# Kernel optimization log

Measured on AMD Instinct MI355X. Metric: run time of the kernel, lower is better.

The kernel has to match this reference:

```python
import jax, jax.numpy as jnp
import numpy as np

B, C, H, W = 4, 256, 64, 64
INTER = C // 2
BN_EPS = 1e-5


def setup_inputs() -> dict:
    key = jax.random.key(0)
    ks = jax.random.split(key, 12)
    s = 0.05
    return {
        "x": jax.random.normal(ks[0], (B, C, H, W), dtype=jnp.float32),
        "theta_w": jax.random.normal(ks[1], (INTER, C), dtype=jnp.float32) * s,
        "theta_b": jax.random.normal(ks[2], (INTER,), dtype=jnp.float32) * s,
        "phi_w": jax.random.normal(ks[3], (INTER, C), dtype=jnp.float32) * s,
        "phi_b": jax.random.normal(ks[4], (INTER,), dtype=jnp.float32) * s,
        "g_w": jax.random.normal(ks[5], (INTER, C), dtype=jnp.float32) * s,
        "g_b": jax.random.normal(ks[6], (INTER,), dtype=jnp.float32) * s,
        "W_w": jax.random.normal(ks[7], (C, INTER), dtype=jnp.float32) * s,
        "W_b": jax.random.normal(ks[8], (C,), dtype=jnp.float32) * s,
        "bn_gamma": jnp.ones((C,), dtype=jnp.float32),
        "bn_beta": jnp.zeros((C,), dtype=jnp.float32),
    }


def _conv1x1(x, w, b):
    # 1x1 conv == per-pixel GEMM: (B,C,H,W) x (O,C) -> (B,O,H,W)
    return jnp.einsum("bchw,oc->bohw", x, w) + b[None, :, None, None]


def reference(x, theta_w, theta_b, phi_w, phi_b, g_w, g_b, W_w, W_b, bn_gamma, bn_beta):
    b, c, h, w = x.shape
    hw = h * w
    theta = _conv1x1(x, theta_w, theta_b).reshape(b, -1, hw)  # (B, inter, HW) -> queries
    phi = _conv1x1(x, phi_w, phi_b).reshape(b, -1, hw)        # (B, inter, HW) -> keys
    g = _conv1x1(x, g_w, g_b).reshape(b, -1, hw)              # (B, inter, HW) -> values
    # f[n,m] = <theta[:,n], phi[:,m]> over all HW spatial positions
    f = jnp.einsum("bin,bim->bnm", theta, phi)                # (B, HW, HW)
    attn = jax.nn.softmax(f, axis=-1)
    y = jnp.einsum("bnm,bim->bin", attn, g)                   # (B, inter, HW)
    y = y.reshape(b, c // 2, h, w)
    wy = _conv1x1(y, W_w, W_b)                                # (B, C, H, W)
    # BatchNorm2d (training-mode batch statistics, per channel)
    mean = jnp.mean(wy, axis=(0, 2, 3), keepdims=True)
    var = jnp.var(wy, axis=(0, 2, 3), keepdims=True)
    wy_bn = bn_gamma[None, :, None, None] * (wy - mean) * jax.lax.rsqrt(var + BN_EPS) + bn_beta[None, :, None, None]
    return wy_bn + x
```

## Files before the change

kernel.cpp:

```cpp
#include <hip/hip_runtime.h>
#include <hip/hip_bf16.h>

#define HWN   4096
#define CIN   256
#define NINTER 128
#define NBATCH 4
#define BN_EPS 1e-5f
#define NC    4
#define CHUNK 1024
#define LOG2E 1.4426950408889634f
#define SMAX  64.0f

typedef __bf16 bf16_t;
typedef __bf16 bf16x8 __attribute__((ext_vector_type(8)));
typedef __bf16 bf16x4 __attribute__((ext_vector_type(4)));
typedef float  f32x4  __attribute__((ext_vector_type(4)));
typedef float  f32x16 __attribute__((ext_vector_type(16)));

__device__ __forceinline__ float fexp2(float x) {
  return __builtin_amdgcn_exp2f(x);
}

#define OFF_QH  0
#define OFF_KH  4194304
#define OFF_V   8388608
#define OFF_YH  12582912
#define OFF_OP  16777216
#define OFF_WY  16777216
#define OFF_LP  50331648
#define OFF_WBF 50855936
#define OFF_ST  51380224

__device__ __forceinline__ void split_bf16(float v, bf16_t& h, bf16_t& l) {
  h = (bf16_t)v;
  l = (bf16_t)(v - (float)h);
}

__global__ __launch_bounds__(256) void convert_weights(
    const float* __restrict__ tw, const float* __restrict__ pw,
    const float* __restrict__ gw, const float* __restrict__ ww,
    bf16_t* __restrict__ out) {
  int i = blockIdx.x * 256 + threadIdx.x;
  float v;
  if (i < 32768)        v = tw[i];
  else if (i < 65536)   v = pw[i - 32768];
  else if (i < 98304)   v = gw[i - 65536];
  else                  v = ww[i - 98304];
  bf16_t h, l;
  split_bf16(v, h, l);
  out[i] = h;
  out[131072 + i] = l;
}

__global__ __launch_bounds__(256, 4) void qkv_kernel(
    const float* __restrict__ x, const bf16_t* __restrict__ wbf,
    const float* __restrict__ tb, const float* __restrict__ pb,
    const float* __restrict__ gb,
    bf16_t* __restrict__ Qh, bf16_t* __restrict__ Kh, bf16_t* __restrict__ V) {
  const int ntb  = blockIdx.x;
  const int b    = blockIdx.y;
  const int tid  = threadIdx.x;
  const int lane = tid & 63;
  const int wv   = tid >> 6;
  const int l31  = lane & 31;
  const int half = lane >> 5;

  __shared__ __align__(16) bf16_t smem[4608];
  bf16_t (*xTh)[72] = (bf16_t(*)[72])smem;
  bf16_t (*xTl)[72] = (bf16_t(*)[72])(smem + 2304);
  bf16_t (*Tr)[136] = (bf16_t(*)[136])smem;

  const bf16_t* Th = wbf;
  const bf16_t* Tl = wbf + 131072;
  const bf16_t* Ph = wbf + 32768;
  const bf16_t* Pl = wbf + 131072 + 32768;
  const bf16_t* Gh = wbf + 65536;
  const float*  xb = x + (size_t)b * CIN * HWN + ntb * 32;

  f32x16 aq, ak, av;
#pragma unroll
  for (int i = 0; i < 16; i++) { aq[i] = 0.f; ak[i] = 0.f; av[i] = 0.f; }

  for (int c0 = 0; c0 < 256; c0 += 64) {
    __syncthreads();
#pragma unroll
    for (int i = 0; i < 8; i++) {
      int idx = tid + i * 256;
      int cc = idx >> 5;
      int nn = idx & 31;
      float v = xb[(size_t)(c0 + cc) * HWN + nn];
      bf16_t h, l;
      split_bf16(v, h, l);
      xTh[nn][cc] = h;
      xTl[nn][cc] = l;
    }
    __syncthreads();
#pragma unroll
    for (int kk = 0; kk < 64; kk += 16) {
      size_t woff = (size_t)(32 * wv + l31) * 256 + c0 + kk + half * 8;
      bf16x8 th = *(const bf16x8*)(Th + woff);
      bf16x8 tl = *(const bf16x8*)(Tl + woff);
      bf16x8 ph = *(const bf16x8*)(Ph + woff);
      bf16x8 pl = *(const bf16x8*)(Pl + woff);
      bf16x8 gh = *(const bf16x8*)(Gh + woff);
      bf16x8 bh = *(const bf16x8*)(&xTh[l31][kk + half * 8]);
      bf16x8 bl = *(const bf16x8*)(&xTl[l31][kk + half * 8]);
      aq = __builtin_amdgcn_mfma_f32_32x32x16_bf16(th, bh, aq, 0, 0, 0);
      aq = __builtin_amdgcn_mfma_f32_32x32x16_bf16(th, bl, aq, 0, 0, 0);
      aq = __builtin_amdgcn_mfma_f32_32x32x16_bf16(tl, bh, aq, 0, 0, 0);
      ak = __builtin_amdgcn_mfma_f32_32x32x16_bf16(ph, bh, ak, 0, 0, 0);
      ak = __builtin_amdgcn_mfma_f32_32x32x16_bf16(ph, bl, ak, 0, 0, 0);
      ak = __builtin_amdgcn_mfma_f32_32x32x16_bf16(pl, bh, ak, 0, 0, 0);
      av = __builtin_amdgcn_mfma_f32_32x32x16_bf16(gh, bh, av, 0, 0, 0);
    }
  }

  const int trow = tid >> 3;
  const int tc16 = (tid & 7) * 16;
  bf16_t* qh = Qh + ((size_t)b * HWN + ntb * 32) * NINTER;
  bf16_t* kh = Kh + ((size_t)b * HWN + ntb * 32) * NINTER;

#pragma unroll
  for (int rnd = 0; rnd < 2; rnd++) {
    __syncthreads();
#pragma unroll
    for (int rg = 0; rg < 4; rg++) {
      int och0 = 32 * wv + 8 * rg + 4 * half;
#pragma unroll
      for (int j = 0; j < 4; j++) {
        float v = (rnd == 0) ? (aq[rg * 4 + j] + tb[och0 + j]) * LOG2E
                             : (ak[rg * 4 + j] + pb[och0 + j]);
        Tr[l31][och0 + j] = (bf16_t)v;
      }
    }
    __syncthreads();
    bf16_t* dst = (rnd == 0) ? qh : kh;
    bf16x8 v0 = *(const bf16x8*)(&Tr[trow][tc16]);
    bf16x8 v1 = *(const bf16x8*)(&Tr[trow][tc16 + 8]);
    *(bf16x8*)(dst + (size_t)trow * NINTER + tc16) = v0;
    *(bf16x8*)(dst + (size_t)trow * NINTER + tc16 + 8) = v1;
  }

  const int n = ntb * 32 + l31;
  bf16_t* vd = V + (size_t)b * NINTER * HWN;
#pragma unroll
  for (int r = 0; r < 16; r++) {
    int och = 32 * wv + (r & 3) + 8 * (r >> 2) + 4 * half;
    vd[(size_t)och * HWN + n] = (bf16_t)(av[r] + gb[och]);
  }
}

__global__ __launch_bounds__(256, 2) void attn_kernel(
    const bf16_t* __restrict__ Qh, const bf16_t* __restrict__ Kh,
    const bf16_t* __restrict__ V,
    float* __restrict__ Opart, float* __restrict__ Lp) {
  const int qt    = blockIdx.x;
  const int chunk = blockIdx.y;
  const int b     = blockIdx.z;
  const int tid   = threadIdx.x;
  const int lane  = tid & 63;
  const int wv    = tid >> 6;
  const int l15   = lane & 15;
  const int quad  = lane >> 4;
  const int kbase = chunk * CHUNK;

  __shared__ __align__(16) bf16_t Klds[32][136];
  __shared__ __align__(16) bf16_t Vlds[144][56];
  __shared__ __align__(16) bf16_t Plds[4][32][40];

  const bf16_t* Qhb = Qh + (size_t)b * HWN * NINTER;
  const bf16_t* Khb = Kh + (size_t)b * HWN * NINTER;
  const bf16_t* Vb  = V + (size_t)b * NINTER * HWN;

  if (tid < 112) {
    int row = 128 + tid / 7;
    int c8 = (tid % 7) * 8;
    bf16x8 v;
#pragma unroll
    for (int j = 0; j < 8; j++) v[j] = (bf16_t)((row == 128) ? 1.0f : 0.0f);
    *(bf16x8*)(&Vlds[row][c8]) = v;
  }

  bf16x8 qf[2][4];
#pragma unroll
  for (int qs = 0; qs < 2; qs++) {
    const int qrow = qt * 128 + wv * 32 + qs * 16 + l15;
#pragma unroll
    for (int kc = 0; kc < 4; kc++)
      qf[qs][kc] = *(const bf16x8*)(Qhb + (size_t)qrow * NINTER + kc * 32 + quad * 8);
  }

  f32x4 o[2][8], ol[2];
#pragma unroll
  for (int qs = 0; qs < 2; qs++) {
#pragma unroll
    for (int dt = 0; dt < 8; dt++)
#pragma unroll
      for (int i = 0; i < 4; i++) o[qs][dt][i] = 0.f;
#pragma unroll
    for (int i = 0; i < 4; i++) ol[qs][i] = 0.f;
  }

  for (int t = 0; t < 32; t++) {
    __syncthreads();
#pragma unroll
    for (int i = 0; i < 2; i++) {
      int idx = tid + i * 256;
      int row = idx >> 4;
      int c8 = (idx & 15) * 8;
      *(uint4*)(&Klds[row][c8]) =
          *(const uint4*)(Khb + (size_t)(kbase + t * 32 + row) * NINTER + c8);
    }
#pragma unroll
    for (int i = 0; i < 2; i++) {
      int idx = tid + i * 256;
      int row = idx >> 2;
      int c8 = (idx & 3) * 8;
      *(uint4*)(&Vlds[row][c8]) =
          *(const uint4*)(Vb + (size_t)row * HWN + kbase + t * 32 + c8);
    }
    __syncthreads();

    f32x4 s[2][2];
#pragma unroll
    for (int qs = 0; qs < 2; qs++)
#pragma unroll
      for (int ks = 0; ks < 2; ks++)
#pragma unroll
        for (int i = 0; i < 4; i++) s[qs][ks][i] = 0.f;
#pragma unroll
    for (int ks = 0; ks < 2; ks++)
#pragma unroll
      for (int kc = 0; kc < 4; kc++) {
        bf16x8 kf = *(const bf16x8*)(&Klds[ks * 16 + l15][kc * 32 + quad * 8]);
        s[0][ks] = __builtin_amdgcn_mfma_f32_16x16x32_bf16(qf[0][kc], kf, s[0][ks], 0, 0, 0);
        s[1][ks] = __builtin_amdgcn_mfma_f32_16x16x32_bf16(qf[1][kc], kf, s[1][ks], 0, 0, 0);
      }

#pragma unroll
    for (int qs = 0; qs < 2; qs++)
#pragma unroll
      for (int ks = 0; ks < 2; ks++)
#pragma unroll
        for (int r = 0; r < 4; r++)
          Plds[wv][qs * 16 + quad * 4 + r][ks * 16 + l15] =
              (bf16_t)fexp2(s[qs][ks][r] - SMAX);

    bf16x8 pf0 = *(const bf16x8*)(&Plds[wv][l15][quad * 8]);
    bf16x8 pf1 = *(const bf16x8*)(&Plds[wv][16 + l15][quad * 8]);
#pragma unroll
    for (int dt = 0; dt < 8; dt++) {
      bf16x8 vf = *(const bf16x8*)(&Vlds[dt * 16 + l15][quad * 8]);
      o[0][dt] = __builtin_amdgcn_mfma_f32_16x16x32_bf16(pf0, vf, o[0][dt], 0, 0, 0);
      o[1][dt] = __builtin_amdgcn_mfma_f32_16x16x32_bf16(pf1, vf, o[1][dt], 0, 0, 0);
    }
    bf16x8 vfl = *(const bf16x8*)(&Vlds[128 + l15][quad * 8]);
    ol[0] = __builtin_amdgcn_mfma_f32_16x16x32_bf16(pf0, vfl, ol[0], 0, 0, 0);
    ol[1] = __builtin_amdgcn_mfma_f32_16x16x32_bf16(pf1, vfl, ol[1], 0, 0, 0);
  }

  float* Ob = Opart + ((size_t)(b * NC + chunk) * HWN) * NINTER;
#pragma unroll
  for (int qs = 0; qs < 2; qs++)
#pragma unroll
    for (int r = 0; r < 4; r++) {
      int n = qt * 128 + wv * 32 + qs * 16 + quad * 4 + r;
#pragma unroll
      for (int dt = 0; dt < 8; dt++)
        Ob[(size_t)n * NINTER + dt * 16 + l15] = o[qs][dt][r];
      if (l15 == 0)
        Lp[(size_t)(b * NC + chunk) * HWN + n] = ol[qs][r];
    }
}

__global__ __launch_bounds__(256, 4) void attn_combine(
    const float* __restrict__ Opart, const float* __restrict__ Lp,
    bf16_t* __restrict__ Yh) {
  int gid = blockIdx.x * 256 + threadIdx.x;
  int d8 = gid & 15;
  int n = (gid >> 4) & 4095;
  int b = gid >> 16;

  float lsum = 0.f;
  float acc[8];
#pragma unroll
  for (int j = 0; j < 8; j++) acc[j] = 0.f;
  const f32x4* Op4 = (const f32x4*)Opart;
#pragma unroll
  for (int c = 0; c < NC; c++) {
    lsum += Lp[(size_t)(b * NC + c) * HWN + n];
    f32x4 o0 = Op4[((size_t)(b * NC + c) * HWN + n) * 32 + d8 * 2];
    f32x4 o1 = Op4[((size_t)(b * NC + c) * HWN + n) * 32 + d8 * 2 + 1];
#pragma unroll
    for (int j = 0; j < 4; j++) { acc[j] += o0[j]; acc[4 + j] += o1[j]; }
  }
  float inv = 1.f / lsum;
  bf16x8 y8;
#pragma unroll
  for (int j = 0; j < 8; j++) y8[j] = (bf16_t)(acc[j] * inv);
  *(bf16x8*)(Yh + ((size_t)b * HWN + n) * NINTER + d8 * 8) = y8;
}

__global__ __launch_bounds__(256, 4) void wconv_kernel(
    const bf16_t* __restrict__ Wbf, const bf16_t* __restrict__ Yp,
    const float* __restrict__ Wb, bf16_t* __restrict__ WY) {
  const int ntb = blockIdx.x;
  const int b   = blockIdx.y;
  const int tid = threadIdx.x;
  const int lane = tid & 63;
  const int wv   = tid >> 6;
  const int l31  = lane & 31;
  const int half = lane >> 5;

  const bf16_t* Wh = Wbf + 98304;
  const bf16_t* Yr = Yp + (size_t)b * HWN * NINTER + (size_t)ntb * 32 * NINTER;

  f32x16 acc[2];
#pragma unroll
  for (int c = 0; c < 2; c++)
#pragma unroll
    for (int i = 0; i < 16; i++) acc[c][i] = 0.f;

#pragma unroll
  for (int k0 = 0; k0 < 128; k0 += 16) {
    bf16x8 a0 = *(const bf16x8*)(Wh + (size_t)(wv * 64 + l31) * NINTER + k0 + half * 8);
    bf16x8 a1 = *(const bf16x8*)(Wh + (size_t)(wv * 64 + 32 + l31) * NINTER + k0 + half * 8);
    bf16x8 b0 = *(const bf16x8*)(Yr + (size_t)l31 * NINTER + k0 + half * 8);
    acc[0] = __builtin_amdgcn_mfma_f32_32x32x16_bf16(a0, b0, acc[0], 0, 0, 0);
    acc[1] = __builtin_amdgcn_mfma_f32_32x32x16_bf16(a1, b0, acc[1], 0, 0, 0);
  }

  bf16_t* dst = WY + (size_t)b * 256 * HWN + ntb * 32;
#pragma unroll
  for (int ct = 0; ct < 2; ct++)
#pragma unroll
    for (int r = 0; r < 16; r++) {
      int co = wv * 64 + ct * 32 + (r & 3) + 8 * (r >> 2) + 4 * half;
      dst[(size_t)co * HWN + l31] = (bf16_t)(acc[ct][r] + Wb[co]);
    }
}

__global__ __launch_bounds__(256) void stats_kernel(
    const bf16_t* __restrict__ WY, float* __restrict__ stats) {
  const int c = blockIdx.x;
  const int tid = threadIdx.x;
  float s = 0.f, s2 = 0.f;
  for (int b = 0; b < NBATCH; b++) {
    const bf16_t* p = WY + ((size_t)b * 256 + c) * HWN;
    for (int i = tid * 8; i < HWN; i += 2048) {
      bf16x8 v8 = *(const bf16x8*)(p + i);
#pragma unroll
      for (int j = 0; j < 8; j++) {
        float v = (float)v8[j];
        s += v;
        s2 += v * v;
      }
    }
  }
#pragma unroll
  for (int off = 1; off < 64; off <<= 1) {
    s += __shfl_xor(s, off);
    s2 += __shfl_xor(s2, off);
  }
  __shared__ float red[8];
  int wv = tid >> 6;
  if ((tid & 63) == 0) { red[wv] = s; red[4 + wv] = s2; }
  __syncthreads();
  if (tid == 0) {
    float S = red[0] + red[1] + red[2] + red[3];
    float S2 = red[4] + red[5] + red[6] + red[7];
    float mean = S * (1.f / 16384.f);
    float var = S2 * (1.f / 16384.f) - mean * mean;
    stats[c] = mean;
    stats[256 + c] = rsqrtf(var + BN_EPS);
  }
}

__global__ __launch_bounds__(256) void bn_kernel(
    const bf16_t* __restrict__ WY, const float* __restrict__ x,
    const float* __restrict__ stats, const float* __restrict__ gamma,
    const float* __restrict__ beta, float* __restrict__ out) {
  int idx = blockIdx.x * 256 + threadIdx.x;
  int e = idx * 4;
  int c = (e >> 12) & 255;
  bf16x4 w4 = *(const bf16x4*)(WY + e);
  float4 xv = *(const float4*)(x + e);
  float mean = stats[c];
  float g = gamma[c] * stats[256 + c];
  float bb = beta[c];
  float4 o;
  o.x = g * ((float)w4[0] - mean) + bb + xv.x;
  o.y = g * ((float)w4[1] - mean) + bb + xv.y;
  o.z = g * ((float)w4[2] - mean) + bb + xv.z;
  o.w = g * ((float)w4[3] - mean) + bb + xv.w;
  *(float4*)(out + e) = o;
}

extern "C" void kernel_launch(void* const* d_in, const int* in_sizes, int n_in,
                              void* d_out, int out_size, void* d_ws, size_t ws_size,
                              hipStream_t stream) {
  const float* x       = (const float*)d_in[0];
  const float* theta_b = (const float*)d_in[2];
  const float* phi_b   = (const float*)d_in[4];
  const float* g_b     = (const float*)d_in[6];
  const float* W_b     = (const float*)d_in[8];
  const float* bn_g    = (const float*)d_in[9];
  const float* bn_b    = (const float*)d_in[10];
  float* out = (float*)d_out;

  char* ws = (char*)d_ws;
  bf16_t* Qh  = (bf16_t*)(ws + OFF_QH);
  bf16_t* Kh  = (bf16_t*)(ws + OFF_KH);
  bf16_t* V   = (bf16_t*)(ws + OFF_V);
  bf16_t* Yh  = (bf16_t*)(ws + OFF_YH);
  float*  OP  = (float*)(ws + OFF_OP);
  bf16_t* WY  = (bf16_t*)(ws + OFF_WY);
  float*  LP  = (float*)(ws + OFF_LP);
  bf16_t* WBF = (bf16_t*)(ws + OFF_WBF);
  float*  ST  = (float*)(ws + OFF_ST);

  convert_weights<<<512, 256, 0, stream>>>(
      (const float*)d_in[1], (const float*)d_in[3],
      (const float*)d_in[5], (const float*)d_in[7], WBF);
  qkv_kernel<<<dim3(128, NBATCH), 256, 0, stream>>>(
      x, WBF, theta_b, phi_b, g_b, Qh, Kh, V);
  attn_kernel<<<dim3(32, NC, NBATCH), 256, 0, stream>>>(
      Qh, Kh, V, OP, LP);
  attn_combine<<<1024, 256, 0, stream>>>(OP, LP, Yh);
  wconv_kernel<<<dim3(128, NBATCH), 256, 0, stream>>>(WBF, Yh, W_b, WY);
  stats_kernel<<<256, 256, 0, stream>>>(WY, ST);
  bn_kernel<<<4096, 256, 0, stream>>>(WY, x, ST, bn_g, bn_b, out);
}
```

Measured before the change: 187.7 us.

## Fuse weight conversion, attention combine and BN stats into neighbouring kernels

Drops the separate weight-conversion kernel; qkv and wconv now read fp32 weights and split or convert them to bf16 inline. The attention partial-sum combine moves into wconv through an LDS tile, and the BN statistics are accumulated with atomics in wconv's epilogue, so bn_kernel derives mean and variance itself. This removes three launches and the Yh and stats round trips through memory. The cost is redundant weight conversion in every block, per-row shuffle reductions with many atomics, and atomic ordering that is not deterministic.

```diff
diff --git a/kernel.cpp b/kernel.cpp
--- a/kernel.cpp
+++ b/kernel.cpp
@@ -21,42 +21,52 @@
   return __builtin_amdgcn_exp2f(x);
 }
 
+__device__ __forceinline__ void split_bf16(float v, bf16_t& h, bf16_t& l) {
+  h = (bf16_t)v;
+  l = (bf16_t)(v - (float)h);
+}
+
+__device__ __forceinline__ void load_split8(const float* p, bf16x8& h, bf16x8& l) {
+  f32x4 a = *(const f32x4*)p;
+  f32x4 b = *(const f32x4*)(p + 4);
+#pragma unroll
+  for (int j = 0; j < 4; j++) {
+    bf16_t hh, ll;
+    split_bf16(a[j], hh, ll);
+    h[j] = hh; l[j] = ll;
+    split_bf16(b[j], hh, ll);
+    h[4 + j] = hh; l[4 + j] = ll;
+  }
+}
+
+__device__ __forceinline__ bf16x8 load_cvt8(const float* p) {
+  f32x4 a = *(const f32x4*)p;
+  f32x4 b = *(const f32x4*)(p + 4);
+  bf16x8 r;
+#pragma unroll
+  for (int j = 0; j < 4; j++) {
+    r[j] = (bf16_t)a[j];
+    r[4 + j] = (bf16_t)b[j];
+  }
+  return r;
+}
+
 #define OFF_QH  0
 #define OFF_KH  4194304
 #define OFF_V   8388608
-#define OFF_YH  12582912
-#define OFF_OP  16777216
-#define OFF_WY  16777216
-#define OFF_LP  50331648
-#define OFF_WBF 50855936
-#define OFF_ST  51380224
-
-__device__ __forceinline__ void split_bf16(float v, bf16_t& h, bf16_t& l) {
-  h = (bf16_t)v;
-  l = (bf16_t)(v - (float)h);
-}
-
-__global__ __launch_bounds__(256) void convert_weights(
+#define OFF_OP  12582912
+#define OFF_WY  46137344
+#define OFF_LP  54525952
+#define OFF_ST  54788096
+
+__global__ __launch_bounds__(256, 4) void qkv_kernel(
+    const float* __restrict__ x,
     const float* __restrict__ tw, const float* __restrict__ pw,
-    const float* __restrict__ gw, const float* __restrict__ ww,
-    bf16_t* __restrict__ out) {
-  int i = blockIdx.x * 256 + threadIdx.x;
-  float v;
-  if (i < 32768)        v = tw[i];
-  else if (i < 65536)   v = pw[i - 32768];
-  else if (i < 98304)   v = gw[i - 65536];
-  else                  v = ww[i - 98304];
-  bf16_t h, l;
-  split_bf16(v, h, l);
-  out[i] = h;
-  out[131072 + i] = l;
-}
-
-__global__ __launch_bounds__(256, 4) void qkv_kernel(
-    const float* __restrict__ x, const bf16_t* __restrict__ wbf,
+    const float* __restrict__ gw,
     const float* __restrict__ tb, const float* __restrict__ pb,
     const float* __restrict__ gb,
-    bf16_t* __restrict__ Qh, bf16_t* __restrict__ Kh, bf16_t* __restrict__ V) {
+    bf16_t* __restrict__ Qh, bf16_t* __restrict__ Kh, bf16_t* __restrict__ V,
+    float* __restrict__ ST) {
   const int ntb  = blockIdx.x;
   const int b    = blockIdx.y;
   const int tid  = threadIdx.x;
@@ -65,17 +75,14 @@
   const int l31  = lane & 31;
   const int half = lane >> 5;
 
+  if (ntb == 0 && b == 0 && tid < 512) ST[tid] = 0.f;
+
   __shared__ __align__(16) bf16_t smem[4608];
   bf16_t (*xTh)[72] = (bf16_t(*)[72])smem;
   bf16_t (*xTl)[72] = (bf16_t(*)[72])(smem + 2304);
   bf16_t (*Tr)[136] = (bf16_t(*)[136])smem;
 
-  const bf16_t* Th = wbf;
-  const bf16_t* Tl = wbf + 131072;
-  const bf16_t* Ph = wbf + 32768;
-  const bf16_t* Pl = wbf + 131072 + 32768;
-  const bf16_t* Gh = wbf + 65536;
-  const float*  xb = x + (size_t)b * CIN * HWN + ntb * 32;
+  const float* xb = x + (size_t)b * CIN * HWN + ntb * 32;
 
   f32x16 aq, ak, av;
 #pragma unroll
@@ -98,11 +105,10 @@
 #pragma unroll
     for (int kk = 0; kk < 64; kk += 16) {
       size_t woff = (size_t)(32 * wv + l31) * 256 + c0 + kk + half * 8;
-      bf16x8 th = *(const bf16x8*)(Th + woff);
-      bf16x8 tl = *(const bf16x8*)(Tl + woff);
-      bf16x8 ph = *(const bf16x8*)(Ph + woff);
-      bf16x8 pl = *(const bf16x8*)(Pl + woff);
-      bf16x8 gh = *(const bf16x8*)(Gh + woff);
+      bf16x8 th, tl, ph, pl;
+      load_split8(tw + woff, th, tl);
+      load_split8(pw + woff, ph, pl);
+      bf16x8 gh = load_cvt8(gw + woff);
       bf16x8 bh = *(const bf16x8*)(&xTh[l31][kk + half * 8]);
       bf16x8 bl = *(const bf16x8*)(&xTl[l31][kk + half * 8]);
       aq = __builtin_amdgcn_mfma_f32_32x32x16_bf16(th, bh, aq, 0, 0, 0);
@@ -273,37 +279,10 @@
     }
 }
 
-__global__ __launch_bounds__(256, 4) void attn_combine(
-    const float* __restrict__ Opart, const float* __restrict__ Lp,
-    bf16_t* __restrict__ Yh) {
-  int gid = blockIdx.x * 256 + threadIdx.x;
-  int d8 = gid & 15;
-  int n = (gid >> 4) & 4095;
-  int b = gid >> 16;
-
-  float lsum = 0.f;
-  float acc[8];
-#pragma unroll
-  for (int j = 0; j < 8; j++) acc[j] = 0.f;
-  const f32x4* Op4 = (const f32x4*)Opart;
-#pragma unroll
-  for (int c = 0; c < NC; c++) {
-    lsum += Lp[(size_t)(b * NC + c) * HWN + n];
-    f32x4 o0 = Op4[((size_t)(b * NC + c) * HWN + n) * 32 + d8 * 2];
-    f32x4 o1 = Op4[((size_t)(b * NC + c) * HWN + n) * 32 + d8 * 2 + 1];
-#pragma unroll
-    for (int j = 0; j < 4; j++) { acc[j] += o0[j]; acc[4 + j] += o1[j]; }
-  }
-  float inv = 1.f / lsum;
-  bf16x8 y8;
-#pragma unroll
-  for (int j = 0; j < 8; j++) y8[j] = (bf16_t)(acc[j] * inv);
-  *(bf16x8*)(Yh + ((size_t)b * HWN + n) * NINTER + d8 * 8) = y8;
-}
-
 __global__ __launch_bounds__(256, 4) void wconv_kernel(
-    const bf16_t* __restrict__ Wbf, const bf16_t* __restrict__ Yp,
-    const float* __restrict__ Wb, bf16_t* __restrict__ WY) {
+    const float* __restrict__ ww, const float* __restrict__ Opart,
+    const float* __restrict__ Lp, const float* __restrict__ Wb,
+    bf16_t* __restrict__ WY, float* __restrict__ ST) {
   const int ntb = blockIdx.x;
   const int b   = blockIdx.y;
   const int tid = threadIdx.x;
@@ -312,8 +291,46 @@
   const int l31  = lane & 31;
   const int half = lane >> 5;
 
-  const bf16_t* Wh = Wbf + 98304;
-  const bf16_t* Yr = Yp + (size_t)b * HWN * NINTER + (size_t)ntb * 32 * NINTER;
+  __shared__ __align__(16) bf16_t Ylds[32][136];
+  __shared__ float Linv[32];
+
+  if (tid < 32) {
+    int n = ntb * 32 + tid;
+    float ls = 0.f;
+#pragma unroll
+    for (int c = 0; c < NC; c++) ls += Lp[(size_t)(b * NC + c) * HWN + n];
+    Linv[tid] = 1.f / ls;
+  }
+
+  const int nrow = tid >> 3;
+  const int dgrp = tid & 7;
+  float oacc[16];
+#pragma unroll
+  for (int j = 0; j < 16; j++) oacc[j] = 0.f;
+#pragma unroll
+  for (int c = 0; c < NC; c++) {
+    const float* Op = Opart +
+        ((size_t)(b * NC + c) * HWN + ntb * 32 + nrow) * NINTER + dgrp * 16;
+#pragma unroll
+    for (int q = 0; q < 4; q++) {
+      f32x4 v = *(const f32x4*)(Op + q * 4);
+#pragma unroll
+      for (int j = 0; j < 4; j++) oacc[q * 4 + j] += v[j];
+    }
+  }
+  __syncthreads();
+  {
+    float inv = Linv[nrow];
+    bf16x8 y0, y1;
+#pragma unroll
+    for (int j = 0; j < 8; j++) {
+      y0[j] = (bf16_t)(oacc[j] * inv);
+      y1[j] = (bf16_t)(oacc[8 + j] * inv);
+    }
+    *(bf16x8*)(&Ylds[nrow][dgrp * 16]) = y0;
+    *(bf16x8*)(&Ylds[nrow][dgrp * 16 + 8]) = y1;
+  }
+  __syncthreads();
 
   f32x16 acc[2];
 #pragma unroll
@@ -323,9 +340,9 @@
 
 #pragma unroll
   for (int k0 = 0; k0 < 128; k0 += 16) {
-    bf16x8 a0 = *(const bf16x8*)(Wh + (size_t)(wv * 64 + l31) * NINTER + k0 + half * 8);
-    bf16x8 a1 = *(const bf16x8*)(Wh + (size_t)(wv * 64 + 32 + l31) * NINTER + k0 + half * 8);
-    bf16x8 b0 = *(const bf16x8*)(Yr + (size_t)l31 * NINTER + k0 + half * 8);
+    bf16x8 a0 = load_cvt8(ww + (size_t)(wv * 64 + l31) * NINTER + k0 + half * 8);
+    bf16x8 a1 = load_cvt8(ww + (size_t)(wv * 64 + 32 + l31) * NINTER + k0 + half * 8);
+    bf16x8 b0 = *(const bf16x8*)(&Ylds[l31][k0 + half * 8]);
     acc[0] = __builtin_amdgcn_mfma_f32_32x32x16_bf16(a0, b0, acc[0], 0, 0, 0);
     acc[1] = __builtin_amdgcn_mfma_f32_32x32x16_bf16(a1, b0, acc[1], 0, 0, 0);
   }
@@ -336,57 +353,34 @@
 #pragma unroll
     for (int r = 0; r < 16; r++) {
       int co = wv * 64 + ct * 32 + (r & 3) + 8 * (r >> 2) + 4 * half;
-      dst[(size_t)co * HWN + l31] = (bf16_t)(acc[ct][r] + Wb[co]);
-    }
-}
-
-__global__ __launch_bounds__(256) void stats_kernel(
-    const bf16_t* __restrict__ WY, float* __restrict__ stats) {
-  const int c = blockIdx.x;
-  const int tid = threadIdx.x;
-  float s = 0.f, s2 = 0.f;
-  for (int b = 0; b < NBATCH; b++) {
-    const bf16_t* p = WY + ((size_t)b * 256 + c) * HWN;
-    for (int i = tid * 8; i < HWN; i += 2048) {
-      bf16x8 v8 = *(const bf16x8*)(p + i);
-#pragma unroll
-      for (int j = 0; j < 8; j++) {
-        float v = (float)v8[j];
-        s += v;
-        s2 += v * v;
+      float v = acc[ct][r] + Wb[co];
+      dst[(size_t)co * HWN + l31] = (bf16_t)v;
+      float s = v, s2 = v * v;
+#pragma unroll
+      for (int off = 1; off < 32; off <<= 1) {
+        s += __shfl_xor(s, off);
+        s2 += __shfl_xor(s2, off);
       }
-    }
-  }
-#pragma unroll
-  for (int off = 1; off < 64; off <<= 1) {
-    s += __shfl_xor(s, off);
-    s2 += __shfl_xor(s2, off);
-  }
-  __shared__ float red[8];
-  int wv = tid >> 6;
-  if ((tid & 63) == 0) { red[wv] = s; red[4 + wv] = s2; }
-  __syncthreads();
-  if (tid == 0) {
-    float S = red[0] + red[1] + red[2] + red[3];
-    float S2 = red[4] + red[5] + red[6] + red[7];
-    float mean = S * (1.f / 16384.f);
-    float var = S2 * (1.f / 16384.f) - mean * mean;
-    stats[c] = mean;
-    stats[256 + c] = rsqrtf(var + BN_EPS);
-  }
+      if (l31 == 0) {
+        atomicAdd(&ST[co], s);
+        atomicAdd(&ST[256 + co], s2);
+      }
+    }
 }
 
 __global__ __launch_bounds__(256) void bn_kernel(
     const bf16_t* __restrict__ WY, const float* __restrict__ x,
-    const float* __restrict__ stats, const float* __restrict__ gamma,
+    const float* __restrict__ ST, const float* __restrict__ gamma,
     const float* __restrict__ beta, float* __restrict__ out) {
   int idx = blockIdx.x * 256 + threadIdx.x;
   int e = idx * 4;
   int c = (e >> 12) & 255;
   bf16x4 w4 = *(const bf16x4*)(WY + e);
   float4 xv = *(const float4*)(x + e);
-  float mean = stats[c];
-  float g = gamma[c] * stats[256 + c];
+  float S = ST[c], S2 = ST[256 + c];
+  float mean = S * (1.f / 16384.f);
+  float var = S2 * (1.f / 16384.f) - mean * mean;
+  float g = gamma[c] * rsqrtf(var + BN_EPS);
   float bb = beta[c];
   float4 o;
   o.x = g * ((float)w4[0] - mean) + bb + xv.x;
@@ -400,9 +394,13 @@
                               void* d_out, int out_size, void* d_ws, size_t ws_size,
                               hipStream_t stream) {
   const float* x       = (const float*)d_in[0];
+  const float* theta_w = (const float*)d_in[1];
   const float* theta_b = (const float*)d_in[2];
+  const float* phi_w   = (const float*)d_in[3];
   const float* phi_b   = (const float*)d_in[4];
+  const float* g_w     = (const float*)d_in[5];
   const float* g_b     = (const float*)d_in[6];
+  const float* W_w     = (const float*)d_in[7];
   const float* W_b     = (const float*)d_in[8];
   const float* bn_g    = (const float*)d_in[9];
   const float* bn_b    = (const float*)d_in[10];
@@ -412,22 +410,16 @@
   bf16_t* Qh  = (bf16_t*)(ws + OFF_QH);
   bf16_t* Kh  = (bf16_t*)(ws + OFF_KH);
   bf16_t* V   = (bf16_t*)(ws + OFF_V);
-  bf16_t* Yh  = (bf16_t*)(ws + OFF_YH);
   float*  OP  = (float*)(ws + OFF_OP);
   bf16_t* WY  = (bf16_t*)(ws + OFF_WY);
   float*  LP  = (float*)(ws + OFF_LP);
-  bf16_t* WBF = (bf16_t*)(ws + OFF_WBF);
   float*  ST  = (float*)(ws + OFF_ST);
 
-  convert_weights<<<512, 256, 0, stream>>>(
-      (const float*)d_in[1], (const float*)d_in[3],
-      (const float*)d_in[5], (const float*)d_in[7], WBF);
   qkv_kernel<<<dim3(128, NBATCH), 256, 0, stream>>>(
-      x, WBF, theta_b, phi_b, g_b, Qh, Kh, V);
+      x, theta_w, phi_w, g_w, theta_b, phi_b, g_b, Qh, Kh, V, ST);
   attn_kernel<<<dim3(32, NC, NBATCH), 256, 0, stream>>>(
       Qh, Kh, V, OP, LP);
-  attn_combine<<<1024, 256, 0, stream>>>(OP, LP, Yh);
-  wconv_kernel<<<dim3(128, NBATCH), 256, 0, stream>>>(WBF, Yh, W_b, WY);
-  stats_kernel<<<256, 256, 0, stream>>>(WY, ST);
+  wconv_kernel<<<dim3(128, NBATCH), 256, 0, stream>>>(
+      W_w, OP, LP, W_b, WY, ST);
   bn_kernel<<<4096, 256, 0, stream>>>(WY, x, ST, bn_g, bn_b, out);
 }
```

Result: slower. 328.8 us (+75.2%).
